# Kernel tuning notes

Measured on AMD Instinct MI355X. Metric: run time of the kernel, lower is better.

## Reference

```python
import jax, jax.numpy as jnp
import numpy as np

G, N, E = 64, 1000, 8192          # graphs, nodes/graph, edges/graph
F_IN, C, H, HID, NCLS = 128, 128, 4, 256, 2
EPS = 1e-5


def _gcn(x, src, dst, W, b):
    # GCNConv: symmetric normalization with self-loops, sum aggregation.
    h = x @ W                                              # [N, C]
    deg = jax.ops.segment_sum(jnp.ones(E, h.dtype), dst, num_segments=N) + 1.0
    dinv = jax.lax.rsqrt(deg)                              # deg^{-1/2}
    msg = h[src] * (dinv[src] * dinv[dst])[:, None]        # [E, C] gather
    out = jax.ops.segment_sum(msg, dst, num_segments=N)    # scatter-add
    out = out + h * (dinv * dinv)[:, None]                 # self-loop term
    return out + b


def _layernorm(y, g, b):
    mu = y.mean(-1, keepdims=True)
    var = ((y - mu) ** 2).mean(-1, keepdims=True)
    return (y - mu) * jax.lax.rsqrt(var + EPS) * g + b


def setup_inputs() -> dict:
    key = jax.random.key(0)
    ks = jax.random.split(key, 12)
    rn = lambda k, s: jax.random.normal(k, s, jnp.float32) * 0.05
    return dict(
        x=jax.random.normal(ks[0], (G, N, F_IN), jnp.float32),
        edge_index=jax.random.randint(ks[1], (G, 2, E), 0, N),
        W0=rn(ks[2], (F_IN, C)), b0=jnp.zeros((C,), jnp.float32),
        W1=rn(ks[3], (C, C)), b1=jnp.zeros((C,), jnp.float32),
        in_w=rn(ks[4], (3 * C, C)), in_b=jnp.zeros((3 * C,), jnp.float32),
        out_w=rn(ks[5], (C, C)), out_b=jnp.zeros((C,), jnp.float32),
        ln2_g=jnp.ones((C,), jnp.float32), ln2_b=jnp.zeros((C,), jnp.float32),
        mw1=rn(ks[6], (C, HID)), mb1=jnp.zeros((HID,), jnp.float32),
        mw2=rn(ks[7], (HID, C)), mb2=jnp.zeros((C,), jnp.float32),
        lw=rn(ks[8], (C, NCLS)), lb=jnp.zeros((NCLS,), jnp.float32),
    )


def reference(x, edge_index, W0, b0, W1, b1, in_w, in_b, out_w, out_b,
              ln2_g, ln2_b, mw1, mb1, mw2, mb2, lw, lb):
    src, dst = edge_index[:, 0, :], edge_index[:, 1, :]
    conv = jax.vmap(_gcn, in_axes=(0, 0, 0, None, None))
    h = jnp.tanh(conv(x, src, dst, W0, b0))   # [G, N, C]
    h = jnp.tanh(conv(h, src, dst, W1, b1))
    g = h.sum(axis=1)                          # SumAggregation -> [G, C]

    # MultiheadAttention, unbatched: sequence of G graph embeddings
    qkv = g @ in_w.T + in_b
    q, k, v = jnp.split(qkv, 3, axis=-1)
    d = C // H
    qh, kh, vh = (t.reshape(G, H, d) for t in (q, k, v))
    attn = jax.nn.softmax(jnp.einsum('qhd,khd->hqk', qh, kh) * (d ** -0.5), axis=-1)
    o = jnp.einsum('hqk,khd->qhd', attn, vh).reshape(G, C) @ out_w.T + out_b

    x_attend = o                               # dropout = identity (eval)
    # NOTE: original computes layer_norm1(x_attend) but immediately overwrites it.
    mlp = jnp.maximum(x_attend @ mw1 + mb1, 0.0) @ mw2 + mb2
    y = _layernorm(x_attend + mlp, ln2_g, ln2_b)
    node_repr = jnp.maximum(y, 0.0).sum(axis=0)  # [C]
    return node_repr @ lw + lb                   # [NCLS]
```

## Files before the change

kernel.cpp:

```cpp
#include <hip/hip_runtime.h>
#include <math.h>

#define Gn 64
#define Nn 1000
#define En 8192
#define Cc 128
#define HIDn 256
#define EPSf 1e-5f

typedef __attribute__((ext_vector_type(8))) short bh8;
typedef __attribute__((ext_vector_type(4))) float fx4;

__device__ __forceinline__ unsigned short f2bf(float f) {
    unsigned u = __float_as_uint(f);
    u += 0x7fffu + ((u >> 16) & 1u);
    return (unsigned short)(u >> 16);
}
__device__ __forceinline__ float bflo(unsigned u) { return __uint_as_float(u << 16); }
__device__ __forceinline__ float bfhi(unsigned u) { return __uint_as_float(u & 0xffff0000u); }

__global__ __launch_bounds__(1024) void k_prep(const int* __restrict__ ei, int* __restrict__ offs,
                                               int* __restrict__ degg, float* __restrict__ selfw,
                                               int2* __restrict__ epair, float* __restrict__ pooled)
{
    __shared__ int degs[1024];
    __shared__ int sb[1024];
    __shared__ int cur[1024];
    __shared__ float dinv_s[1024];
    int g = blockIdx.x, t = threadIdx.x;
    const int* srcp = ei + (size_t)g * 2 * En;
    const int* dstp = srcp + En;
    degs[t] = 0;
    __syncthreads();
    for (int e = t; e < En; e += 1024) atomicAdd(&degs[dstp[e]], 1);
    __syncthreads();
    int d = (t < Nn) ? degs[t] : 0;
    sb[t] = d;
    __syncthreads();
    for (int st = 1; st < 1024; st <<= 1) {
        int v2 = (t >= st) ? sb[t - st] : 0;
        __syncthreads();
        sb[t] += v2;
        __syncthreads();
    }
    int ex = sb[t] - d;
    float dv = rsqrtf((float)d + 1.0f);
    cur[t] = ex;
    dinv_s[t] = dv;
    if (t < Nn) {
        offs[g * Nn + t] = ex;
        degg[g * Nn + t] = d;
        selfw[g * Nn + t] = dv * dv;
    }
    __syncthreads();
    for (int e = t; e < En; e += 1024) {
        int dd = dstp[e], ss = srcp[e];
        int p = atomicAdd(&cur[dd], 1);
        float w = dinv_s[ss] * dinv_s[dd];
        epair[(size_t)g * En + p] = make_int2(ss, __float_as_int(w));
    }
    if (t < Cc) pooled[g * Cc + t] = 0.f;
}

template<int INBF>
__global__ __launch_bounds__(256) void k_gemm(const void* __restrict__ Xin, const float* __restrict__ W,
                                              unsigned short* __restrict__ Hout)
{
    __shared__ __align__(16) short Wt[128][136];
    int b = blockIdx.x;
    int xcd = b & 7, j = b >> 3;
    int g = xcd + 8 * (j & 7);
    int rblk = j >> 3;
    int t = threadIdx.x;
    for (int idx = t; idx < 16384; idx += 256) {
        int kI = idx >> 7, n = idx & 127;
        Wt[n][kI] = (short)f2bf(W[idx]);
    }
    __syncthreads();
    int wave = t >> 6, l = t & 63;
    int lr = l & 15, lg = l >> 4;
    const float* Xf = (const float*)Xin + (size_t)g * Nn * Cc;
    const short* Xh = (const short*)Xin + (size_t)g * Nn * Cc;
    unsigned short* Hg = Hout + (size_t)g * Nn * Cc;

    for (int s = 0; s < 4; ++s) {
        int rbase = rblk * 256 + wave * 64 + s * 16;
        int r = rbase + lr;
        bool ok = r < Nn;
        bh8 af[4];
        if (INBF) {
            #pragma unroll
            for (int ks = 0; ks < 4; ++ks) {
                if (ok) af[ks] = *(const bh8*)(Xh + (size_t)r * Cc + ks * 32 + lg * 8);
                else    af[ks] = bh8{0, 0, 0, 0, 0, 0, 0, 0};
            }
        } else {
            #pragma unroll
            for (int ks = 0; ks < 4; ++ks) {
                if (ok) {
                    const float* xp = Xf + (size_t)r * Cc + ks * 32 + lg * 8;
                    fx4 a0 = *(const fx4*)xp;
                    fx4 a1 = *(const fx4*)(xp + 4);
                    bh8 av;
                    av[0] = (short)f2bf(a0[0]); av[1] = (short)f2bf(a0[1]);
                    av[2] = (short)f2bf(a0[2]); av[3] = (short)f2bf(a0[3]);
                    av[4] = (short)f2bf(a1[0]); av[5] = (short)f2bf(a1[1]);
                    av[6] = (short)f2bf(a1[2]); av[7] = (short)f2bf(a1[3]);
                    af[ks] = av;
                } else af[ks] = bh8{0, 0, 0, 0, 0, 0, 0, 0};
            }
        }
        fx4 acc[8];
        #pragma unroll
        for (int ct = 0; ct < 8; ++ct) acc[ct] = fx4{0.f, 0.f, 0.f, 0.f};
        #pragma unroll
        for (int ks = 0; ks < 4; ++ks) {
            #pragma unroll
            for (int ct = 0; ct < 8; ++ct) {
                bh8 bfr = *(const bh8*)(&Wt[ct * 16 + lr][ks * 32 + lg * 8]);
                acc[ct] = __builtin_amdgcn_mfma_f32_16x16x32_bf16(af[ks], bfr, acc[ct], 0, 0, 0);
            }
        }
        #pragma unroll
        for (int ct = 0; ct < 8; ++ct) {
            #pragma unroll
            for (int rg = 0; rg < 4; ++rg) {
                int row = rbase + lg * 4 + rg;
                if (row < Nn) Hg[(size_t)row * Cc + ct * 16 + lr] = f2bf(acc[ct][rg]);
            }
        }
    }
}

template<int POOL>
__global__ __launch_bounds__(256) void k_combine(const unsigned* __restrict__ Hb, const int2* __restrict__ epair,
                                                 const int* __restrict__ offs, const int* __restrict__ degg,
                                                 const float* __restrict__ selfw, const float* __restrict__ bias,
                                                 unsigned* __restrict__ Tout, float* __restrict__ pooled)
{
    int b = blockIdx.x;
    int xcd = b & 7, j = b >> 3;
    int g = xcd + 8 * (j & 7);
    int blk = j >> 3;
    int wave = threadIdx.x >> 6, lane = threadIdx.x & 63;
    const unsigned* Hg = Hb + (size_t)g * Nn * 64;
    const int2* epg = epair + (size_t)g * En;
    float2 bb = *(const float2*)(bias + lane * 2);
    float px = 0.f, py = 0.f;
    for (int n = blk * 4 + wave; n < Nn; n += 128) {
        float sw = selfw[g * Nn + n];
        int st = offs[g * Nn + n];
        int dc = degg[g * Nn + n];
        unsigned hv = Hg[n * 64 + lane];
        float ax = bflo(hv) * sw + bb.x;
        float ay = bfhi(hv) * sw + bb.y;
        float bx = 0.f, by = 0.f;
        int e = 0;
        for (; e + 2 <= dc; e += 2) {
            int2 p0 = epg[st + e];
            int2 p1 = epg[st + e + 1];
            unsigned r0 = Hg[p0.x * 64 + lane];
            unsigned r1 = Hg[p1.x * 64 + lane];
            float w0 = __int_as_float(p0.y), w1 = __int_as_float(p1.y);
            ax = fmaf(bflo(r0), w0, ax); ay = fmaf(bfhi(r0), w0, ay);
            bx = fmaf(bflo(r1), w1, bx); by = fmaf(bfhi(r1), w1, by);
        }
        if (e < dc) {
            int2 p0 = epg[st + e];
            unsigned r0 = Hg[p0.x * 64 + lane];
            float w0 = __int_as_float(p0.y);
            ax = fmaf(bflo(r0), w0, ax); ay = fmaf(bfhi(r0), w0, ay);
        }
        ax += bx; ay += by;
        float tx = tanhf(ax), ty = tanhf(ay);
        if (POOL) { px += tx; py += ty; }
        else Tout[(size_t)(g * Nn + n) * 64 + lane] = ((unsigned)f2bf(ty) << 16) | (unsigned)f2bf(tx);
    }
    if (POOL) {
        atomicAdd(&pooled[g * Cc + lane * 2], px);
        atomicAdd(&pooled[g * Cc + lane * 2 + 1], py);
    }
}

__global__ __launch_bounds__(1024) void k_qkv(const float* __restrict__ pooled, const float* __restrict__ in_w,
                                              const float* __restrict__ in_b, float* __restrict__ qkvb,
                                              float* __restrict__ repr)
{
    int t = threadIdx.x, lane = t & 63, wv = t >> 6;
    int c = blockIdx.x * 16 + wv;
    if (blockIdx.x == 0 && t < Cc) repr[t] = 0.f;
    const float* wr = in_w + c * Cc;
    float w0 = wr[lane], w1 = wr[64 + lane];
    float bias = in_b[c];
    for (int i = 0; i < Gn; ++i) {
        float p = fmaf(pooled[i * Cc + lane], w0, pooled[i * Cc + 64 + lane] * w1);
        #pragma unroll
        for (int off2 = 32; off2 > 0; off2 >>= 1) p += __shfl_xor(p, off2);
        if (lane == 0) qkvb[i * 384 + c] = p + bias;
    }
}

__global__ __launch_bounds__(1024) void k_attn(const float* __restrict__ qkvb, float* __restrict__ ob)
{
    __shared__ float q[64][33], kk[64][33], v[64][33];
    __shared__ float S[64][64];
    int h = blockIdx.x, t = threadIdx.x;

    for (int idx = t; idx < 2048; idx += 1024) {
        int i = idx >> 5, cc = idx & 31;
        q[i][cc]  = qkvb[i * 384 + h * 32 + cc];
        kk[i][cc] = qkvb[i * 384 + 128 + h * 32 + cc];
        v[i][cc]  = qkvb[i * 384 + 256 + h * 32 + cc];
    }
    __syncthreads();

    for (int idx = t; idx < 4096; idx += 1024) {
        int i = idx >> 6, jj = idx & 63;
        float acc = 0.f;
        #pragma unroll
        for (int d2 = 0; d2 < 32; ++d2) acc = fmaf(q[i][d2], kk[jj][d2], acc);
        S[i][jj] = acc * 0.17677669529663687f;
    }
    __syncthreads();

    int lane = t & 63, w = t >> 6;
    for (int r = w; r < 64; r += 16) {
        float val = S[r][lane];
        float m = val;
        #pragma unroll
        for (int off = 32; off > 0; off >>= 1) m = fmaxf(m, __shfl_xor(m, off));
        float e2 = expf(val - m);
        float ssum = e2;
        #pragma unroll
        for (int off = 32; off > 0; off >>= 1) ssum += __shfl_xor(ssum, off);
        S[r][lane] = e2 / ssum;
    }
    __syncthreads();

    for (int idx = t; idx < 2048; idx += 1024) {
        int i = idx >> 5, d2 = idx & 31;
        float acc = 0.f;
        #pragma unroll 4
        for (int k2 = 0; k2 < 64; ++k2) acc = fmaf(S[i][k2], v[k2][d2], acc);
        ob[i * Cc + h * 32 + d2] = acc;
    }
}

__global__ __launch_bounds__(1024) void k_tail(const float* __restrict__ ob, const float* __restrict__ out_w,
                                               const float* __restrict__ out_b, const float* __restrict__ mw1,
                                               const float* __restrict__ mb1, const float* __restrict__ mw2,
                                               const float* __restrict__ mb2, const float* __restrict__ ln2g,
                                               const float* __restrict__ ln2b, float* __restrict__ repr)
{
    __shared__ float sob[4][128];
    __shared__ float sxatt[4][128];
    __shared__ float sm1[4][256];
    __shared__ float spart[4][128];
    __shared__ float pr[128];
    int g0 = blockIdx.x * 4;
    int t = threadIdx.x, lane = t & 63, wv = t >> 6;

    if (t < 512) sob[t >> 7][t & 127] = ob[(size_t)(g0 + (t >> 7)) * Cc + (t & 127)];
    if (t < 128) pr[t] = 0.f;
    __syncthreads();

    for (int c = wv; c < Cc; c += 16) {
        float w0 = out_w[c * Cc + lane];
        float w1 = out_w[c * Cc + 64 + lane];
        float bc = out_b[c];
        #pragma unroll
        for (int g = 0; g < 4; ++g) {
            float p = fmaf(sob[g][lane], w0, sob[g][64 + lane] * w1);
            #pragma unroll
            for (int off = 32; off > 0; off >>= 1) p += __shfl_xor(p, off);
            if (lane == 0) sxatt[g][c] = p + bc;
        }
    }
    __syncthreads();

    {
        int j = t & 255, gi = t >> 8;
        float acc = mb1[j];
        #pragma unroll 8
        for (int k = 0; k < Cc; ++k) acc = fmaf(sxatt[gi][k], mw1[k * HIDn + j], acc);
        sm1[gi][j] = fmaxf(acc, 0.f);
    }
    __syncthreads();

    {
        int c = t & 127, gi = (t >> 7) & 3, half = t >> 9;
        int k0 = half * 128;
        float acc = 0.f;
        #pragma unroll 8
        for (int k = 0; k < 128; ++k) acc = fmaf(sm1[gi][k0 + k], mw2[(k0 + k) * Cc + c], acc);
        if (half) spart[gi][c] = acc;
        __syncthreads();
        if (!half) sxatt[gi][c] = sxatt[gi][c] + acc + spart[gi][c] + mb2[c];
    }
    __syncthreads();

    if (t < 256) {
        int g = wv;
        float v0 = sxatt[g][lane], v1 = sxatt[g][64 + lane];
        float s = v0 + v1;
        #pragma unroll
        for (int off = 32; off > 0; off >>= 1) s += __shfl_xor(s, off);
        float mu = s * (1.f / 128.f);
        float d0 = v0 - mu, d1 = v1 - mu;
        float vv = d0 * d0 + d1 * d1;
        #pragma unroll
        for (int off = 32; off > 0; off >>= 1) vv += __shfl_xor(vv, off);
        float rstd = rsqrtf(vv * (1.f / 128.f) + EPSf);
        float z0 = fmaxf(d0 * rstd * ln2g[lane] + ln2b[lane], 0.f);
        float z1 = fmaxf(d1 * rstd * ln2g[64 + lane] + ln2b[64 + lane], 0.f);
        atomicAdd(&pr[lane], z0);
        atomicAdd(&pr[64 + lane], z1);
    }
    __syncthreads();
    if (t < 128) atomicAdd(&repr[t], pr[t]);
}

__global__ __launch_bounds__(128) void k_final(const float* __restrict__ repr, const float* __restrict__ lw,
                                               const float* __restrict__ lb, float* __restrict__ out)
{
    __shared__ float r0[Cc], r1[Cc];
    int t = threadIdx.x;
    float r = repr[t];
    r0[t] = r * lw[t * 2 + 0];
    r1[t] = r * lw[t * 2 + 1];
    __syncthreads();
    for (int s2 = 64; s2 > 0; s2 >>= 1) {
        if (t < s2) { r0[t] += r0[t + s2]; r1[t] += r1[t + s2]; }
        __syncthreads();
    }
    if (t == 0) {
        out[0] = r0[0] + lb[0];
        out[1] = r1[0] + lb[1];
    }
}

extern "C" void kernel_launch(void* const* d_in, const int* in_sizes, int n_in,
                              void* d_out, int out_size, void* d_ws, size_t ws_size,
                              hipStream_t stream)
{
    const float* x     = (const float*)d_in[0];
    const int*   ei    = (const int*)d_in[1];
    const float* W0    = (const float*)d_in[2];
    const float* b0    = (const float*)d_in[3];
    const float* W1    = (const float*)d_in[4];
    const float* b1    = (const float*)d_in[5];
    const float* in_w  = (const float*)d_in[6];
    const float* in_b  = (const float*)d_in[7];
    const float* out_w = (const float*)d_in[8];
    const float* out_b = (const float*)d_in[9];
    const float* ln2g  = (const float*)d_in[10];
    const float* ln2b  = (const float*)d_in[11];
    const float* mw1   = (const float*)d_in[12];
    const float* mb1   = (const float*)d_in[13];
    const float* mw2   = (const float*)d_in[14];
    const float* mb2   = (const float*)d_in[15];
    const float* lw    = (const float*)d_in[16];
    const float* lb    = (const float*)d_in[17];
    float* out = (float*)d_out;
    (void)in_sizes; (void)n_in; (void)out_size; (void)ws_size;

    char* ws = (char*)d_ws;
    size_t off = 0;
    auto carve = [&](size_t bytes) { size_t o = off; off += (bytes + 255) & ~(size_t)255; return o; };
    size_t o_offs  = carve((size_t)Gn * Nn * 4);
    size_t o_deg   = carve((size_t)Gn * Nn * 4);
    size_t o_selfw = carve((size_t)Gn * Nn * 4);
    size_t o_ep    = carve((size_t)Gn * En * 8);
    size_t o_pool  = carve((size_t)Gn * Cc * 4);
    size_t o_qkv   = carve((size_t)Gn * 384 * 4);
    size_t o_ob    = carve((size_t)Gn * Cc * 4);
    size_t o_repr  = carve((size_t)Cc * 4);
    size_t o_H     = carve((size_t)Gn * Nn * Cc * 2);
    size_t o_T     = carve((size_t)Gn * Nn * Cc * 2);

    int*   offs   = (int*)(ws + o_offs);
    int*   degg   = (int*)(ws + o_deg);
    float* selfw  = (float*)(ws + o_selfw);
    int2*  epair  = (int2*)(ws + o_ep);
    float* pooled = (float*)(ws + o_pool);
    float* qkvb   = (float*)(ws + o_qkv);
    float* ob     = (float*)(ws + o_ob);
    float* repr   = (float*)(ws + o_repr);
    unsigned short* H = (unsigned short*)(ws + o_H);
    unsigned short* T = (unsigned short*)(ws + o_T);

    k_prep<<<Gn, 1024, 0, stream>>>(ei, offs, degg, selfw, epair, pooled);
    k_gemm<0><<<256, 256, 0, stream>>>(x, W0, H);
    k_combine<0><<<2048, 256, 0, stream>>>((const unsigned*)H, epair, offs, degg, selfw, b0, (unsigned*)T, nullptr);
    k_gemm<1><<<256, 256, 0, stream>>>(T, W1, H);
    k_combine<1><<<2048, 256, 0, stream>>>((const unsigned*)H, epair, offs, degg, selfw, b1, nullptr, pooled);
    k_qkv<<<24, 1024, 0, stream>>>(pooled, in_w, in_b, qkvb, repr);
    k_attn<<<4, 1024, 0, stream>>>(qkvb, ob);
    k_tail<<<16, 1024, 0, stream>>>(ob, out_w, out_b, mw1, mb1, mw2, mb2, ln2g, ln2b, repr);
    k_final<<<1, 128, 0, stream>>>(repr, lw, lb, out);
}
```

Baseline: 175.1 us.

## Merge prep with first GEMM, pack node info, unroll gather, fuse final

Runs graph preprocessing and the first feature GEMM in one launch, using separate block ranges, so the two independent stages overlap. The first GEMM now uses one 1024-thread block per graph instead of 4 row blocks. Per-node offset, degree and self-weight are packed into one int4 so each is a single load. The edge-gather loop is unrolled to 4 independent accumulators for more memory-level parallelism. The final linear layer is folded into the tail kernel with a last-block atomic counter, removing one launch at the cost of a threadfence and counter logic.

```diff
diff --git a/kernel.cpp b/kernel.cpp
--- a/kernel.cpp
+++ b/kernel.cpp
@@ -19,82 +19,69 @@
 __device__ __forceinline__ float bflo(unsigned u) { return __uint_as_float(u << 16); }
 __device__ __forceinline__ float bfhi(unsigned u) { return __uint_as_float(u & 0xffff0000u); }
 
-__global__ __launch_bounds__(1024) void k_prep(const int* __restrict__ ei, int* __restrict__ offs,
-                                               int* __restrict__ degg, float* __restrict__ selfw,
-                                               int2* __restrict__ epair, float* __restrict__ pooled)
+__global__ __launch_bounds__(1024) void k_pg0(const int* __restrict__ ei, const float* __restrict__ X,
+                                              const float* __restrict__ W, int4* __restrict__ ninfo,
+                                              int2* __restrict__ epair, float* __restrict__ pooled,
+                                              float* __restrict__ repr, int* __restrict__ ctr,
+                                              unsigned short* __restrict__ Hout)
 {
     __shared__ int degs[1024];
     __shared__ int sb[1024];
     __shared__ int cur[1024];
     __shared__ float dinv_s[1024];
-    int g = blockIdx.x, t = threadIdx.x;
-    const int* srcp = ei + (size_t)g * 2 * En;
-    const int* dstp = srcp + En;
-    degs[t] = 0;
-    __syncthreads();
-    for (int e = t; e < En; e += 1024) atomicAdd(&degs[dstp[e]], 1);
-    __syncthreads();
-    int d = (t < Nn) ? degs[t] : 0;
-    sb[t] = d;
-    __syncthreads();
-    for (int st = 1; st < 1024; st <<= 1) {
-        int v2 = (t >= st) ? sb[t - st] : 0;
-        __syncthreads();
-        sb[t] += v2;
-        __syncthreads();
-    }
-    int ex = sb[t] - d;
-    float dv = rsqrtf((float)d + 1.0f);
-    cur[t] = ex;
-    dinv_s[t] = dv;
-    if (t < Nn) {
-        offs[g * Nn + t] = ex;
-        degg[g * Nn + t] = d;
-        selfw[g * Nn + t] = dv * dv;
-    }
-    __syncthreads();
-    for (int e = t; e < En; e += 1024) {
-        int dd = dstp[e], ss = srcp[e];
-        int p = atomicAdd(&cur[dd], 1);
-        float w = dinv_s[ss] * dinv_s[dd];
-        epair[(size_t)g * En + p] = make_int2(ss, __float_as_int(w));
-    }
-    if (t < Cc) pooled[g * Cc + t] = 0.f;
-}
-
-template<int INBF>
-__global__ __launch_bounds__(256) void k_gemm(const void* __restrict__ Xin, const float* __restrict__ W,
-                                              unsigned short* __restrict__ Hout)
-{
     __shared__ __align__(16) short Wt[128][136];
-    int b = blockIdx.x;
-    int xcd = b & 7, j = b >> 3;
-    int g = xcd + 8 * (j & 7);
-    int rblk = j >> 3;
     int t = threadIdx.x;
-    for (int idx = t; idx < 16384; idx += 256) {
-        int kI = idx >> 7, n = idx & 127;
-        Wt[n][kI] = (short)f2bf(W[idx]);
-    }
-    __syncthreads();
-    int wave = t >> 6, l = t & 63;
-    int lr = l & 15, lg = l >> 4;
-    const float* Xf = (const float*)Xin + (size_t)g * Nn * Cc;
-    const short* Xh = (const short*)Xin + (size_t)g * Nn * Cc;
-    unsigned short* Hg = Hout + (size_t)g * Nn * Cc;
-
-    for (int s = 0; s < 4; ++s) {
-        int rbase = rblk * 256 + wave * 64 + s * 16;
-        int r = rbase + lr;
-        bool ok = r < Nn;
-        bh8 af[4];
-        if (INBF) {
-            #pragma unroll
-            for (int ks = 0; ks < 4; ++ks) {
-                if (ok) af[ks] = *(const bh8*)(Xh + (size_t)r * Cc + ks * 32 + lg * 8);
-                else    af[ks] = bh8{0, 0, 0, 0, 0, 0, 0, 0};
-            }
-        } else {
+
+    if (blockIdx.x < 64) {
+        int g = blockIdx.x;
+        const int* srcp = ei + (size_t)g * 2 * En;
+        const int* dstp = srcp + En;
+        degs[t] = 0;
+        __syncthreads();
+        for (int e = t; e < En; e += 1024) atomicAdd(&degs[dstp[e]], 1);
+        __syncthreads();
+        int d = (t < Nn) ? degs[t] : 0;
+        sb[t] = d;
+        __syncthreads();
+        for (int st = 1; st < 1024; st <<= 1) {
+            int v2 = (t >= st) ? sb[t - st] : 0;
+            __syncthreads();
+            sb[t] += v2;
+            __syncthreads();
+        }
+        int ex = sb[t] - d;
+        float dv = rsqrtf((float)d + 1.0f);
+        cur[t] = ex;
+        dinv_s[t] = dv;
+        if (t < Nn) ninfo[g * Nn + t] = make_int4(ex, d, __float_as_int(dv * dv), 0);
+        __syncthreads();
+        for (int e = t; e < En; e += 1024) {
+            int dd = dstp[e], ss = srcp[e];
+            int p = atomicAdd(&cur[dd], 1);
+            float w = dinv_s[ss] * dinv_s[dd];
+            epair[(size_t)g * En + p] = make_int2(ss, __float_as_int(w));
+        }
+        if (t < Cc) pooled[g * Cc + t] = 0.f;
+        if (g == 0 && t < Cc) repr[t] = 0.f;
+        if (g == 0 && t == 0) *ctr = 0;
+    } else {
+        int g = blockIdx.x - 64;
+        for (int idx = t; idx < 16384; idx += 1024) {
+            int kI = idx >> 7, n = idx & 127;
+            Wt[n][kI] = (short)f2bf(W[idx]);
+        }
+        __syncthreads();
+        int wave = t >> 6, l = t & 63;
+        int lr = l & 15, lg = l >> 4;
+        const float* Xf = X + (size_t)g * Nn * Cc;
+        unsigned short* Hg = Hout + (size_t)g * Nn * Cc;
+
+        #pragma unroll
+        for (int s = 0; s < 4; ++s) {
+            int rbase = wave * 64 + s * 16;
+            int r = rbase + lr;
+            bool ok = r < Nn;
+            bh8 af[4];
             #pragma unroll
             for (int ks = 0; ks < 4; ++ks) {
                 if (ok) {
@@ -109,6 +96,58 @@
                     af[ks] = av;
                 } else af[ks] = bh8{0, 0, 0, 0, 0, 0, 0, 0};
             }
+            fx4 acc[8];
+            #pragma unroll
+            for (int ct = 0; ct < 8; ++ct) acc[ct] = fx4{0.f, 0.f, 0.f, 0.f};
+            #pragma unroll
+            for (int ks = 0; ks < 4; ++ks) {
+                #pragma unroll
+                for (int ct = 0; ct < 8; ++ct) {
+                    bh8 bfr = *(const bh8*)(&Wt[ct * 16 + lr][ks * 32 + lg * 8]);
+                    acc[ct] = __builtin_amdgcn_mfma_f32_16x16x32_bf16(af[ks], bfr, acc[ct], 0, 0, 0);
+                }
+            }
+            #pragma unroll
+            for (int ct = 0; ct < 8; ++ct) {
+                #pragma unroll
+                for (int rg = 0; rg < 4; ++rg) {
+                    int row = rbase + lg * 4 + rg;
+                    if (row < Nn) Hg[(size_t)row * Cc + ct * 16 + lr] = f2bf(acc[ct][rg]);
+                }
+            }
+        }
+    }
+}
+
+__global__ __launch_bounds__(256) void k_gemm1(const unsigned short* __restrict__ Xh,
+                                               const float* __restrict__ W,
+                                               unsigned short* __restrict__ Hout)
+{
+    __shared__ __align__(16) short Wt[128][136];
+    int b = blockIdx.x;
+    int xcd = b & 7, j = b >> 3;
+    int g = xcd + 8 * (j & 7);
+    int rblk = j >> 3;
+    int t = threadIdx.x;
+    for (int idx = t; idx < 16384; idx += 256) {
+        int kI = idx >> 7, n = idx & 127;
+        Wt[n][kI] = (short)f2bf(W[idx]);
+    }
+    __syncthreads();
+    int wave = t >> 6, l = t & 63;
+    int lr = l & 15, lg = l >> 4;
+    const short* Xg = (const short*)Xh + (size_t)g * Nn * Cc;
+    unsigned short* Hg = Hout + (size_t)g * Nn * Cc;
+
+    for (int s = 0; s < 4; ++s) {
+        int rbase = rblk * 256 + wave * 64 + s * 16;
+        int r = rbase + lr;
+        bool ok = r < Nn;
+        bh8 af[4];
+        #pragma unroll
+        for (int ks = 0; ks < 4; ++ks) {
+            if (ok) af[ks] = *(const bh8*)(Xg + (size_t)r * Cc + ks * 32 + lg * 8);
+            else    af[ks] = bh8{0, 0, 0, 0, 0, 0, 0, 0};
         }
         fx4 acc[8];
         #pragma unroll
@@ -134,8 +173,7 @@
 
 template<int POOL>
 __global__ __launch_bounds__(256) void k_combine(const unsigned* __restrict__ Hb, const int2* __restrict__ epair,
-                                                 const int* __restrict__ offs, const int* __restrict__ degg,
-                                                 const float* __restrict__ selfw, const float* __restrict__ bias,
+                                                 const int4* __restrict__ ninfo, const float* __restrict__ bias,
                                                  unsigned* __restrict__ Tout, float* __restrict__ pooled)
 {
     int b = blockIdx.x;
@@ -145,33 +183,41 @@
     int wave = threadIdx.x >> 6, lane = threadIdx.x & 63;
     const unsigned* Hg = Hb + (size_t)g * Nn * 64;
     const int2* epg = epair + (size_t)g * En;
+    const int4* nig = ninfo + (size_t)g * Nn;
     float2 bb = *(const float2*)(bias + lane * 2);
     float px = 0.f, py = 0.f;
     for (int n = blk * 4 + wave; n < Nn; n += 128) {
-        float sw = selfw[g * Nn + n];
-        int st = offs[g * Nn + n];
-        int dc = degg[g * Nn + n];
+        int4 ni = nig[n];
+        int st = ni.x, dc = ni.y;
+        float sw = __int_as_float(ni.z);
         unsigned hv = Hg[n * 64 + lane];
-        float ax = bflo(hv) * sw + bb.x;
-        float ay = bfhi(hv) * sw + bb.y;
-        float bx = 0.f, by = 0.f;
+        float a0x = bflo(hv) * sw + bb.x, a0y = bfhi(hv) * sw + bb.y;
+        float a1x = 0.f, a1y = 0.f, a2x = 0.f, a2y = 0.f, a3x = 0.f, a3y = 0.f;
         int e = 0;
-        for (; e + 2 <= dc; e += 2) {
+        for (; e + 4 <= dc; e += 4) {
             int2 p0 = epg[st + e];
             int2 p1 = epg[st + e + 1];
+            int2 p2 = epg[st + e + 2];
+            int2 p3 = epg[st + e + 3];
             unsigned r0 = Hg[p0.x * 64 + lane];
             unsigned r1 = Hg[p1.x * 64 + lane];
+            unsigned r2 = Hg[p2.x * 64 + lane];
+            unsigned r3 = Hg[p3.x * 64 + lane];
             float w0 = __int_as_float(p0.y), w1 = __int_as_float(p1.y);
-            ax = fmaf(bflo(r0), w0, ax); ay = fmaf(bfhi(r0), w0, ay);
-            bx = fmaf(bflo(r1), w1, bx); by = fmaf(bfhi(r1), w1, by);
-        }
-        if (e < dc) {
+            float w2 = __int_as_float(p2.y), w3 = __int_as_float(p3.y);
+            a0x = fmaf(bflo(r0), w0, a0x); a0y = fmaf(bfhi(r0), w0, a0y);
+            a1x = fmaf(bflo(r1), w1, a1x); a1y = fmaf(bfhi(r1), w1, a1y);
+            a2x = fmaf(bflo(r2), w2, a2x); a2y = fmaf(bfhi(r2), w2, a2y);
+            a3x = fmaf(bflo(r3), w3, a3x); a3y = fmaf(bfhi(r3), w3, a3y);
+        }
+        for (; e < dc; ++e) {
             int2 p0 = epg[st + e];
             unsigned r0 = Hg[p0.x * 64 + lane];
             float w0 = __int_as_float(p0.y);
-            ax = fmaf(bflo(r0), w0, ax); ay = fmaf(bfhi(r0), w0, ay);
-        }
-        ax += bx; ay += by;
+            a0x = fmaf(bflo(r0), w0, a0x); a0y = fmaf(bfhi(r0), w0, a0y);
+        }
+        float ax = (a0x + a1x) + (a2x + a3x);
+        float ay = (a0y + a1y) + (a2y + a3y);
         float tx = tanhf(ax), ty = tanhf(ay);
         if (POOL) { px += tx; py += ty; }
         else Tout[(size_t)(g * Nn + n) * 64 + lane] = ((unsigned)f2bf(ty) << 16) | (unsigned)f2bf(tx);
@@ -183,12 +229,10 @@
 }
 
 __global__ __launch_bounds__(1024) void k_qkv(const float* __restrict__ pooled, const float* __restrict__ in_w,
-                                              const float* __restrict__ in_b, float* __restrict__ qkvb,
-                                              float* __restrict__ repr)
+                                              const float* __restrict__ in_b, float* __restrict__ qkvb)
 {
     int t = threadIdx.x, lane = t & 63, wv = t >> 6;
     int c = blockIdx.x * 16 + wv;
-    if (blockIdx.x == 0 && t < Cc) repr[t] = 0.f;
     const float* wr = in_w + c * Cc;
     float w0 = wr[lane], w1 = wr[64 + lane];
     float bias = in_b[c];
@@ -246,17 +290,20 @@
     }
 }
 
-__global__ __launch_bounds__(1024) void k_tail(const float* __restrict__ ob, const float* __restrict__ out_w,
-                                               const float* __restrict__ out_b, const float* __restrict__ mw1,
-                                               const float* __restrict__ mb1, const float* __restrict__ mw2,
-                                               const float* __restrict__ mb2, const float* __restrict__ ln2g,
-                                               const float* __restrict__ ln2b, float* __restrict__ repr)
+__global__ __launch_bounds__(1024) void k_tailfinal(const float* __restrict__ ob, const float* __restrict__ out_w,
+                                                    const float* __restrict__ out_b, const float* __restrict__ mw1,
+                                                    const float* __restrict__ mb1, const float* __restrict__ mw2,
+                                                    const float* __restrict__ mb2, const float* __restrict__ ln2g,
+                                                    const float* __restrict__ ln2b, const float* __restrict__ lw,
+                                                    const float* __restrict__ lb, float* __restrict__ repr,
+                                                    int* __restrict__ ctr, float* __restrict__ out)
 {
     __shared__ float sob[4][128];
     __shared__ float sxatt[4][128];
     __shared__ float sm1[4][256];
     __shared__ float spart[4][128];
     __shared__ float pr[128];
+    __shared__ int slast;
     int g0 = blockIdx.x * 4;
     int t = threadIdx.x, lane = t & 63, wv = t >> 6;
 
@@ -318,24 +365,25 @@
     }
     __syncthreads();
     if (t < 128) atomicAdd(&repr[t], pr[t]);
-}
-
-__global__ __launch_bounds__(128) void k_final(const float* __restrict__ repr, const float* __restrict__ lw,
-                                               const float* __restrict__ lb, float* __restrict__ out)
-{
-    __shared__ float r0[Cc], r1[Cc];
-    int t = threadIdx.x;
-    float r = repr[t];
-    r0[t] = r * lw[t * 2 + 0];
-    r1[t] = r * lw[t * 2 + 1];
-    __syncthreads();
-    for (int s2 = 64; s2 > 0; s2 >>= 1) {
-        if (t < s2) { r0[t] += r0[t + s2]; r1[t] += r1[t + s2]; }
-        __syncthreads();
-    }
-    if (t == 0) {
-        out[0] = r0[0] + lb[0];
-        out[1] = r1[0] + lb[1];
+
+    __threadfence();
+    __syncthreads();
+    if (t == 0) slast = atomicAdd(ctr, 1);
+    __syncthreads();
+    if (slast == 15) {
+        __threadfence();
+        __shared__ float r0s[128], r1s[128];
+        if (t < 128) {
+            float r = __hip_atomic_load(&repr[t], __ATOMIC_RELAXED, __HIP_MEMORY_SCOPE_AGENT);
+            r0s[t] = r * lw[t * 2 + 0];
+            r1s[t] = r * lw[t * 2 + 1];
+        }
+        __syncthreads();
+        for (int s2 = 64; s2 > 0; s2 >>= 1) {
+            if (t < s2) { r0s[t] += r0s[t + s2]; r1s[t] += r1s[t + s2]; }
+            __syncthreads();
+        }
+        if (t == 0) { out[0] = r0s[0] + lb[0]; out[1] = r1s[0] + lb[1]; }
     }
 }
 
@@ -367,35 +415,32 @@
     char* ws = (char*)d_ws;
     size_t off = 0;
     auto carve = [&](size_t bytes) { size_t o = off; off += (bytes + 255) & ~(size_t)255; return o; };
-    size_t o_offs  = carve((size_t)Gn * Nn * 4);
-    size_t o_deg   = carve((size_t)Gn * Nn * 4);
-    size_t o_selfw = carve((size_t)Gn * Nn * 4);
+    size_t o_ni    = carve((size_t)Gn * Nn * 16);
     size_t o_ep    = carve((size_t)Gn * En * 8);
     size_t o_pool  = carve((size_t)Gn * Cc * 4);
     size_t o_qkv   = carve((size_t)Gn * 384 * 4);
     size_t o_ob    = carve((size_t)Gn * Cc * 4);
     size_t o_repr  = carve((size_t)Cc * 4);
+    size_t o_ctr   = carve(256);
     size_t o_H     = carve((size_t)Gn * Nn * Cc * 2);
     size_t o_T     = carve((size_t)Gn * Nn * Cc * 2);
 
-    int*   offs   = (int*)(ws + o_offs);
-    int*   degg   = (int*)(ws + o_deg);
-    float* selfw  = (float*)(ws + o_selfw);
+    int4*  ninfo  = (int4*)(ws + o_ni);
     int2*  epair  = (int2*)(ws + o_ep);
     float* pooled = (float*)(ws + o_pool);
     float* qkvb   = (float*)(ws + o_qkv);
     float* ob     = (float*)(ws + o_ob);
     float* repr   = (float*)(ws + o_repr);
+    int*   ctr    = (int*)(ws + o_ctr);
     unsigned short* H = (unsigned short*)(ws + o_H);
     unsigned short* T = (unsigned short*)(ws + o_T);
 
-    k_prep<<<Gn, 1024, 0, stream>>>(ei, offs, degg, selfw, epair, pooled);
-    k_gemm<0><<<256, 256, 0, stream>>>(x, W0, H);
-    k_combine<0><<<2048, 256, 0, stream>>>((const unsigned*)H, epair, offs, degg, selfw, b0, (unsigned*)T, nullptr);
-    k_gemm<1><<<256, 256, 0, stream>>>(T, W1, H);
-    k_combine<1><<<2048, 256, 0, stream>>>((const unsigned*)H, epair, offs, degg, selfw, b1, nullptr, pooled);
-    k_qkv<<<24, 1024, 0, stream>>>(pooled, in_w, in_b, qkvb, repr);
+    k_pg0<<<128, 1024, 0, stream>>>(ei, x, W0, ninfo, epair, pooled, repr, ctr, H);
+    k_combine<0><<<2048, 256, 0, stream>>>((const unsigned*)H, epair, ninfo, b0, (unsigned*)T, nullptr);
+    k_gemm1<<<256, 256, 0, stream>>>(T, W1, H);
+    k_combine<1><<<2048, 256, 0, stream>>>((const unsigned*)H, epair, ninfo, b1, nullptr, pooled);
+    k_qkv<<<24, 1024, 0, stream>>>(pooled, in_w, in_b, qkvb);
     k_attn<<<4, 1024, 0, stream>>>(qkvb, ob);
-    k_tail<<<16, 1024, 0, stream>>>(ob, out_w, out_b, mw1, mb1, mw2, mb2, ln2g, ln2b, repr);
-    k_final<<<1, 128, 0, stream>>>(repr, lw, lb, out);
-}
+    k_tailfinal<<<16, 1024, 0, stream>>>(ob, out_w, out_b, mw1, mb1, mw2, mb2, ln2g, ln2b,
+                                         lw, lb, repr, ctr, out);
+}
```

New measurement: 182.5 us. 1.04x slower.
